# Kernel optimization log

Measured on AMD Instinct MI355X. Metric: run time of the kernel, lower is better.

Reference implementation:

```python
import jax, jax.numpy as jnp
import numpy as np

EPS = 1e-6


def setup_inputs() -> dict:
    key = jax.random.key(0)
    kx, ky = jax.random.split(key)
    B, C, H, W = 8, 128, 48, 64
    x = jax.random.normal(kx, (B, C, H, W), dtype=jnp.float32)
    y = jax.random.normal(ky, (B, C, H, W), dtype=jnp.float32)
    return {"x": x, "y": y}


def reference(x, y):
    # x, y: (b, c, h, w)
    b, c, h, w = x.shape
    # torch: x.transpose(2,3).view(b,c,h*w) -> x flattened w-major,
    #        so output channel k = v*h + u corresponds to x[:, :, u, v].
    # corr5[b, v, u, i, j] = sum_c x[b,c,u,v] * y[b,c,i,j]
    corr = jnp.einsum('bcuv,bcij->bvuij', x, y)
    corr = corr.reshape(b, w * h, h, w)  # channel k = v*h + u
    # normalization: ReLU then L2-normalize over the h*w channel dim
    corr = jax.nn.relu(corr)
    norm = jnp.sqrt(jnp.sum(corr * corr, axis=1, keepdims=True) + EPS)
    return corr / norm
```

## Files before the change

kernel.cpp:

```cpp
#include <hip/hip_runtime.h>
#include <hip/hip_bf16.h>

#define NB 8
#define NC 128
#define NH 48
#define NW 64
#define NS 3072
#define EPSF 1e-6f

#define GLOBAL_AS __attribute__((address_space(1)))
#define LDS_AS __attribute__((address_space(3)))

typedef __bf16 bf16x8 __attribute__((ext_vector_type(8)));
typedef float f32x4 __attribute__((ext_vector_type(4)));

__global__ __launch_bounds__(256) void transpose_both(
    const float* __restrict__ x, const float* __restrict__ y,
    __hip_bfloat16* __restrict__ AT, __hip_bfloat16* __restrict__ BT) {
  __shared__ float tile[32][65];
  const int id = blockIdx.x;
  const int b = id & 7;
  const int which = (id >> 3) & 1;
  const int rr = id >> 4;
  const int f0 = (rr % 96) * 32, c0 = (rr / 96) * 64;
  const float* src = which ? y : x;
  __hip_bfloat16* dst = which ? BT : AT;
  const int t = threadIdx.x;

  const int fi = t & 31, ci0 = t >> 5;
  const float* sp = src + ((size_t)b * NC + c0) * NS + f0;
#pragma unroll
  for (int i = 0; i < 8; ++i) {
    int ci = ci0 + i * 8;
    tile[fi][ci] = sp[(size_t)ci * NS + fi];
  }
  __syncthreads();

  const int co = t & 63, fo0 = t >> 6;
#pragma unroll
  for (int i = 0; i < 8; ++i) {
    int fo = fo0 + i * 4;
    int f = f0 + fo;
    int k = which ? f : ((f & 63) * NH + (f >> 6));
    dst[((size_t)b * NS + k) * NC + c0 + co] = __float2bfloat16(tile[fo][co]);
  }
}

__device__ __forceinline__ void stage_tile(const char* gsrc, char* ldst,
                                           int wid, int lane) {
  const int lr = lane >> 4, lg = lane & 15;
#pragma unroll
  for (int i = 0; i < 8; ++i) {
    int c = wid * 8 + i;
    int row = c * 4 + lr;
    int g = lg ^ (row & 7);
    __builtin_amdgcn_global_load_lds(
        (const GLOBAL_AS unsigned*)(gsrc + row * 256 + g * 16),
        (LDS_AS unsigned*)(ldst + c * 1024), 16, 0, 0);
  }
}

__device__ __forceinline__ void gemm_step(const char* As, const char* Bs,
                                          float cs[4], int wm, int wn,
                                          int l15, int kg) {
  f32x4 acc[4][4] = {};
  const int rx = l15 & 7;
#pragma unroll
  for (int kk = 0; kk < 4; ++kk) {
    int g = (kk * 4 + kg) ^ rx;
    bf16x8 a[4], bb[4];
#pragma unroll
    for (int mi = 0; mi < 4; ++mi)
      a[mi] = *(const bf16x8*)(As + (wm * 64 + mi * 16 + l15) * 256 + g * 16);
#pragma unroll
    for (int ni = 0; ni < 4; ++ni)
      bb[ni] = *(const bf16x8*)(Bs + (wn * 64 + ni * 16 + l15) * 256 + g * 16);
#pragma unroll
    for (int mi = 0; mi < 4; ++mi)
#pragma unroll
      for (int ni = 0; ni < 4; ++ni)
        acc[mi][ni] = __builtin_amdgcn_mfma_f32_16x16x32_bf16(
            a[mi], bb[ni], acc[mi][ni], 0, 0, 0);
  }
#pragma unroll
  for (int ni = 0; ni < 4; ++ni)
#pragma unroll
    for (int mi = 0; mi < 4; ++mi)
#pragma unroll
      for (int r = 0; r < 4; ++r) {
        float v = fmaxf(acc[mi][ni][r], 0.f);
        cs[ni] += v * v;
      }
}

__global__ __launch_bounds__(256, 1) void corr_norm(
    const __hip_bfloat16* __restrict__ AT,
    const __hip_bfloat16* __restrict__ BT, float* __restrict__ rn) {
  __shared__ char smem[98304];
  char* Bs = smem + 65536;
  const int id = blockIdx.x;
  const int b = id & 7;
  const int nt = id >> 3;
  const int t = threadIdx.x;
  const int lane = t & 63, wid = t >> 6;
  const int wm = wid >> 1, wn = wid & 1;
  const int l15 = lane & 15, kg = lane >> 4;

  const char* Ab = (const char*)(AT + (size_t)b * NS * NC);
  const char* Bg = (const char*)(BT + ((size_t)b * NS + nt * 128) * NC);

  stage_tile(Bg, Bs, wid, lane);
  stage_tile(Ab, smem, wid, lane);
  __syncthreads();

  float cs[4] = {0.f, 0.f, 0.f, 0.f};
#pragma unroll 1
  for (int mt = 0; mt < 24; mt += 2) {
    stage_tile(Ab + (size_t)(mt + 1) * 32768, smem + 32768, wid, lane);
    gemm_step(smem, Bs, cs, wm, wn, l15, kg);
    __syncthreads();
    if (mt + 2 < 24)
      stage_tile(Ab + (size_t)(mt + 2) * 32768, smem, wid, lane);
    gemm_step(smem + 32768, Bs, cs, wm, wn, l15, kg);
    __syncthreads();
  }

#pragma unroll
  for (int ni = 0; ni < 4; ++ni) {
    cs[ni] += __shfl_xor(cs[ni], 16, 64);
    cs[ni] += __shfl_xor(cs[ni], 32, 64);
  }
  float* csum = (float*)smem;
  if (kg == 0) {
#pragma unroll
    for (int ni = 0; ni < 4; ++ni)
      csum[wm * 128 + wn * 64 + ni * 16 + l15] = cs[ni];
  }
  __syncthreads();
  if (t < 128) {
    float s = csum[t] + csum[128 + t];
    rn[(size_t)b * NS + nt * 128 + t] = rsqrtf(s + EPSF);
  }
}

__global__ __launch_bounds__(256, 2) void corr_out(
    const __hip_bfloat16* __restrict__ AT,
    const __hip_bfloat16* __restrict__ BT, const float* __restrict__ rn,
    float* __restrict__ out) {
  __shared__ char smem[66560];
  float* rnc = (float*)(smem + 65536);
  const int id = blockIdx.x;
  const int b = id & 7;
  const int tl = id >> 3;
  const int mt = tl / 24, nt = tl - mt * 24;
  const int t = threadIdx.x;
  const int lane = t & 63, wid = t >> 6;
  const int wm = wid >> 1, wn = wid & 1;
  const int l15 = lane & 15, kg = lane >> 4;

  const char* Ag = (const char*)(AT + ((size_t)b * NS + mt * 128) * NC);
  const char* Bg = (const char*)(BT + ((size_t)b * NS + nt * 128) * NC);
  stage_tile(Ag, smem, wid, lane);
  stage_tile(Bg, smem + 32768, wid, lane);
  if (t < 128) rnc[t] = rn[(size_t)b * NS + nt * 128 + t];
  __syncthreads();

  f32x4 acc[4][4] = {};
  const int rx = l15 & 7;
#pragma unroll
  for (int kk = 0; kk < 4; ++kk) {
    int g = (kk * 4 + kg) ^ rx;
    bf16x8 a[4], bb[4];
#pragma unroll
    for (int mi = 0; mi < 4; ++mi)
      a[mi] = *(const bf16x8*)(smem + (wm * 64 + mi * 16 + l15) * 256 + g * 16);
#pragma unroll
    for (int ni = 0; ni < 4; ++ni)
      bb[ni] = *(const bf16x8*)(smem + 32768 +
                                (wn * 64 + ni * 16 + l15) * 256 + g * 16);
#pragma unroll
    for (int mi = 0; mi < 4; ++mi)
#pragma unroll
      for (int ni = 0; ni < 4; ++ni)
        acc[mi][ni] = __builtin_amdgcn_mfma_f32_16x16x32_bf16(
            a[mi], bb[ni], acc[mi][ni], 0, 0, 0);
  }

  float rnv[4];
#pragma unroll
  for (int ni = 0; ni < 4; ++ni) rnv[ni] = rnc[wn * 64 + ni * 16 + l15];
  __syncthreads();

  float* tf = (float*)smem;
#pragma unroll
  for (int mi = 0; mi < 4; ++mi)
#pragma unroll
    for (int ni = 0; ni < 4; ++ni)
#pragma unroll
      for (int r = 0; r < 4; ++r) {
        int row = wm * 64 + mi * 16 + kg * 4 + r;
        int col = wn * 64 + ni * 16 + l15;
        tf[row * 129 + col] = fmaxf(acc[mi][ni][r], 0.f) * rnv[ni];
      }
  __syncthreads();

  float* ob = out + (size_t)b * NS * NS + (size_t)(mt * 128) * NS + nt * 128;
  const int rsub = t >> 5, c4 = (t & 31) * 4;
#pragma unroll
  for (int it = 0; it < 16; ++it) {
    int row = it * 8 + rsub;
    f32x4 v = *(const f32x4*)&tf[row * 129 + c4];
    __builtin_nontemporal_store(v, (f32x4*)&ob[(size_t)row * NS + c4]);
  }
}

extern "C" void kernel_launch(void* const* d_in, const int* in_sizes, int n_in,
                              void* d_out, int out_size, void* d_ws,
                              size_t ws_size, hipStream_t stream) {
  const float* x = (const float*)d_in[0];
  const float* y = (const float*)d_in[1];
  float* out = (float*)d_out;
  char* ws = (char*)d_ws;

  const size_t AT_OFF = 0;
  const size_t BT_OFF = 6291456;
  const size_t RN_OFF = 12582912;
  const size_t NEED = 12681216;
  if (ws_size < NEED) return;

  __hip_bfloat16* AT = (__hip_bfloat16*)(ws + AT_OFF);
  __hip_bfloat16* BT = (__hip_bfloat16*)(ws + BT_OFF);
  float* rn = (float*)(ws + RN_OFF);

  dim3 tb(256);
  transpose_both<<<dim3(3072), tb, 0, stream>>>(x, y, AT, BT);
  corr_norm<<<dim3(192), tb, 0, stream>>>(AT, BT, rn);
  corr_out<<<dim3(4608), tb, 0, stream>>>(AT, BT, rn, out);
}
```

Baseline: 102.4 us.

## Split norm-pass reduction over M into four partial blocks with 512 threads

The norm pass previously launched only 192 blocks, each looping over all 24 M tiles, which underfills a 256-CU GPU. It now launches 768 blocks of 512 threads (8 waves, each with a 64x32 sub-tile). Each block covers a quarter of the M range and writes partial sums of squares, and corr_out adds the four partials and applies rsqrt. Waits use an explicit vmcnt wait plus s_barrier. In exchange it adds a partial buffer and extra reads in corr_out.

```diff
diff --git a/kernel.cpp b/kernel.cpp
--- a/kernel.cpp
+++ b/kernel.cpp
@@ -46,12 +46,13 @@
   }
 }
 
+template <int CPW>
 __device__ __forceinline__ void stage_tile(const char* gsrc, char* ldst,
                                            int wid, int lane) {
   const int lr = lane >> 4, lg = lane & 15;
 #pragma unroll
-  for (int i = 0; i < 8; ++i) {
-    int c = wid * 8 + i;
+  for (int i = 0; i < CPW; ++i) {
+    int c = wid * CPW + i;
     int row = c * 4 + lr;
     int g = lg ^ (row & 7);
     __builtin_amdgcn_global_load_lds(
@@ -60,30 +61,30 @@
   }
 }
 
-__device__ __forceinline__ void gemm_step(const char* As, const char* Bs,
-                                          float cs[4], int wm, int wn,
-                                          int l15, int kg) {
-  f32x4 acc[4][4] = {};
+__device__ __forceinline__ void gemm_acc(const char* As, const char* Bs,
+                                         float cs[2], int wm, int wn, int l15,
+                                         int kg) {
+  f32x4 acc[4][2] = {};
   const int rx = l15 & 7;
 #pragma unroll
   for (int kk = 0; kk < 4; ++kk) {
     int g = (kk * 4 + kg) ^ rx;
-    bf16x8 a[4], bb[4];
+    bf16x8 a[4], bb[2];
 #pragma unroll
     for (int mi = 0; mi < 4; ++mi)
       a[mi] = *(const bf16x8*)(As + (wm * 64 + mi * 16 + l15) * 256 + g * 16);
 #pragma unroll
-    for (int ni = 0; ni < 4; ++ni)
-      bb[ni] = *(const bf16x8*)(Bs + (wn * 64 + ni * 16 + l15) * 256 + g * 16);
-#pragma unroll
-    for (int mi = 0; mi < 4; ++mi)
-#pragma unroll
-      for (int ni = 0; ni < 4; ++ni)
+    for (int ni = 0; ni < 2; ++ni)
+      bb[ni] = *(const bf16x8*)(Bs + (wn * 32 + ni * 16 + l15) * 256 + g * 16);
+#pragma unroll
+    for (int mi = 0; mi < 4; ++mi)
+#pragma unroll
+      for (int ni = 0; ni < 2; ++ni)
         acc[mi][ni] = __builtin_amdgcn_mfma_f32_16x16x32_bf16(
             a[mi], bb[ni], acc[mi][ni], 0, 0, 0);
   }
 #pragma unroll
-  for (int ni = 0; ni < 4; ++ni)
+  for (int ni = 0; ni < 2; ++ni)
 #pragma unroll
     for (int mi = 0; mi < 4; ++mi)
 #pragma unroll
@@ -93,59 +94,64 @@
       }
 }
 
-__global__ __launch_bounds__(256, 1) void corr_norm(
+__global__ __launch_bounds__(512, 1) void corr_part_p(
     const __hip_bfloat16* __restrict__ AT,
-    const __hip_bfloat16* __restrict__ BT, float* __restrict__ rn) {
+    const __hip_bfloat16* __restrict__ BT, float* __restrict__ part) {
   __shared__ char smem[98304];
   char* Bs = smem + 65536;
   const int id = blockIdx.x;
   const int b = id & 7;
-  const int nt = id >> 3;
+  const int tl = id >> 3;
+  const int nt = tl >> 2, mq = tl & 3;
   const int t = threadIdx.x;
   const int lane = t & 63, wid = t >> 6;
-  const int wm = wid >> 1, wn = wid & 1;
+  const int wm = wid >> 2, wn = wid & 3;
   const int l15 = lane & 15, kg = lane >> 4;
 
-  const char* Ab = (const char*)(AT + (size_t)b * NS * NC);
+  const char* Ab = (const char*)(AT + ((size_t)b * NS + mq * 768) * NC);
   const char* Bg = (const char*)(BT + ((size_t)b * NS + nt * 128) * NC);
 
-  stage_tile(Bg, Bs, wid, lane);
-  stage_tile(Ab, smem, wid, lane);
-  __syncthreads();
-
-  float cs[4] = {0.f, 0.f, 0.f, 0.f};
+  stage_tile<4>(Bg, Bs, wid, lane);
+  stage_tile<4>(Ab, smem, wid, lane);
+  asm volatile("s_waitcnt vmcnt(0)" ::: "memory");
+  __builtin_amdgcn_sched_barrier(0);
+  __builtin_amdgcn_s_barrier();
+
+  float cs[2] = {0.f, 0.f};
+  int cur = 0;
 #pragma unroll 1
-  for (int mt = 0; mt < 24; mt += 2) {
-    stage_tile(Ab + (size_t)(mt + 1) * 32768, smem + 32768, wid, lane);
-    gemm_step(smem, Bs, cs, wm, wn, l15, kg);
-    __syncthreads();
-    if (mt + 2 < 24)
-      stage_tile(Ab + (size_t)(mt + 2) * 32768, smem, wid, lane);
-    gemm_step(smem + 32768, Bs, cs, wm, wn, l15, kg);
-    __syncthreads();
-  }
-
-#pragma unroll
-  for (int ni = 0; ni < 4; ++ni) {
+  for (int i = 0; i < 6; ++i) {
+    if (i + 1 < 6)
+      stage_tile<4>(Ab + (size_t)(i + 1) * 32768, smem + ((cur ^ 1) * 32768),
+                    wid, lane);
+    gemm_acc(smem + cur * 32768, Bs, cs, wm, wn, l15, kg);
+    asm volatile("s_waitcnt vmcnt(0)" ::: "memory");
+    __builtin_amdgcn_sched_barrier(0);
+    __builtin_amdgcn_s_barrier();
+    cur ^= 1;
+  }
+
+#pragma unroll
+  for (int ni = 0; ni < 2; ++ni) {
     cs[ni] += __shfl_xor(cs[ni], 16, 64);
     cs[ni] += __shfl_xor(cs[ni], 32, 64);
   }
   float* csum = (float*)smem;
   if (kg == 0) {
 #pragma unroll
-    for (int ni = 0; ni < 4; ++ni)
-      csum[wm * 128 + wn * 64 + ni * 16 + l15] = cs[ni];
+    for (int ni = 0; ni < 2; ++ni)
+      csum[wm * 128 + wn * 32 + ni * 16 + l15] = cs[ni];
   }
   __syncthreads();
   if (t < 128) {
     float s = csum[t] + csum[128 + t];
-    rn[(size_t)b * NS + nt * 128 + t] = rsqrtf(s + EPSF);
+    part[(size_t)mq * (NB * NS) + (size_t)b * NS + nt * 128 + t] = s;
   }
 }
 
 __global__ __launch_bounds__(256, 2) void corr_out(
     const __hip_bfloat16* __restrict__ AT,
-    const __hip_bfloat16* __restrict__ BT, const float* __restrict__ rn,
+    const __hip_bfloat16* __restrict__ BT, const float* __restrict__ part_in,
     float* __restrict__ out) {
   __shared__ char smem[66560];
   float* rnc = (float*)(smem + 65536);
@@ -160,9 +166,15 @@
 
   const char* Ag = (const char*)(AT + ((size_t)b * NS + mt * 128) * NC);
   const char* Bg = (const char*)(BT + ((size_t)b * NS + nt * 128) * NC);
-  stage_tile(Ag, smem, wid, lane);
-  stage_tile(Bg, smem + 32768, wid, lane);
-  if (t < 128) rnc[t] = rn[(size_t)b * NS + nt * 128 + t];
+  stage_tile<8>(Ag, smem, wid, lane);
+  stage_tile<8>(Bg, smem + 32768, wid, lane);
+  if (t < 128) {
+    float s = 0.f;
+#pragma unroll
+    for (int q = 0; q < 4; ++q)
+      s += part_in[(size_t)q * (NB * NS) + (size_t)b * NS + nt * 128 + t];
+    rnc[t] = rsqrtf(s + EPSF);
+  }
   __syncthreads();
 
   f32x4 acc[4][4] = {};
@@ -224,16 +236,15 @@
 
   const size_t AT_OFF = 0;
   const size_t BT_OFF = 6291456;
-  const size_t RN_OFF = 12582912;
-  const size_t NEED = 12681216;
+  const size_t PART_OFF = 12582912;
+  const size_t NEED = 12976128;
   if (ws_size < NEED) return;
 
   __hip_bfloat16* AT = (__hip_bfloat16*)(ws + AT_OFF);
   __hip_bfloat16* BT = (__hip_bfloat16*)(ws + BT_OFF);
-  float* rn = (float*)(ws + RN_OFF);
-
-  dim3 tb(256);
-  transpose_both<<<dim3(3072), tb, 0, stream>>>(x, y, AT, BT);
-  corr_norm<<<dim3(192), tb, 0, stream>>>(AT, BT, rn);
-  corr_out<<<dim3(4608), tb, 0, stream>>>(AT, BT, rn, out);
-}
+  float* part = (float*)(ws + PART_OFF);
+
+  transpose_both<<<dim3(3072), dim3(256), 0, stream>>>(x, y, AT, BT);
+  corr_part_p<<<dim3(768), dim3(512), 0, stream>>>(AT, BT, part);
+  corr_out<<<dim3(4608), dim3(256), 0, stream>>>(AT, BT, part, out);
+}
```

After: 99.19 us. 3.1% less time.
